# Kernel optimization log

Measured on AMD Instinct MI355X. Metric: run time of the kernel, lower is better.

The kernel has to match this reference:

```python
import jax, jax.numpy as jnp
import numpy as np
from jax import lax

RADIUS = 8
EPS = 1e-3
EPS_LOG = 1e-6
EPS_SCALE = 1e-4
A_COMP = 0.7
B_SHIFT = 0.0
DETAIL_GAIN = 1.0
DOWN = 0.5
# detail_threshold=0 and target_mean=0 -> those branches are inactive (defaults)

DN = (('NCHW', 'OIHW', 'NCHW'))


def _box_filter(x4d):
    """Separable box filter on [1,1,H,W] with reflect padding, kernel 2r+1."""
    k = 2 * RADIUS + 1
    xp = jnp.pad(x4d, ((0, 0), (0, 0), (RADIUS, RADIUS), (RADIUS, RADIUS)), mode='reflect')
    kh = jnp.full((1, 1, 1, k), 1.0 / k, dtype=x4d.dtype)
    kv = jnp.full((1, 1, k, 1), 1.0 / k, dtype=x4d.dtype)
    y = lax.conv_general_dilated(xp, kh, (1, 1), 'VALID', dimension_numbers=DN)
    y = lax.conv_general_dilated(y, kv, (1, 1), 'VALID', dimension_numbers=DN)
    return y


def _guided_filter(img):
    """Self-guided filter on a 2D image [H, W]."""
    x4 = img[None, None]
    mean_I = _box_filter(x4)
    mean_II = _box_filter(x4 * x4)
    var_I = mean_II - mean_I * mean_I
    a = var_I / (var_I + EPS)
    b = mean_I - a * mean_I
    out = _box_filter(a) * x4 + _box_filter(b)
    return out[0, 0]


def _bilinear_resize(img, oh, ow):
    """Bilinear resize [H,W] -> [oh,ow], half-pixel centers (align_corners=False),
    no antialias, matching torch F.interpolate(mode='bilinear')."""
    H, W = img.shape
    ys = jnp.maximum((jnp.arange(oh, dtype=img.dtype) + 0.5) * (H / oh) - 0.5, 0.0)
    xs = jnp.maximum((jnp.arange(ow, dtype=img.dtype) + 0.5) * (W / ow) - 0.5, 0.0)
    y0 = jnp.floor(ys)
    x0 = jnp.floor(xs)
    wy = (ys - y0)[:, None]
    wx = (xs - x0)[None, :]
    y0i = jnp.clip(y0.astype(jnp.int32), 0, H - 1)
    y1i = jnp.minimum(y0i + 1, H - 1)
    x0i = jnp.clip(x0.astype(jnp.int32), 0, W - 1)
    x1i = jnp.minimum(x0i + 1, W - 1)
    # vertical lerp, then horizontal lerp (separable)
    vert = img[y0i, :] * (1.0 - wy) + img[y1i, :] * wy       # [oh, W]
    out = vert[:, x0i] * (1.0 - wx) + vert[:, x1i] * wx      # [oh, ow]
    return out


def setup_inputs() -> dict:
    key = jax.random.key(0)
    x = jax.random.uniform(key, (2160, 3840, 3), dtype=jnp.float32)
    return {"x": x}


def reference(x) -> jnp.ndarray:
    H, W = x.shape[0], x.shape[1]
    Y = 0.2126 * x[..., 0] + 0.7152 * x[..., 1] + 0.0722 * x[..., 2]
    Y_log = jnp.log2(jnp.maximum(Y, EPS_LOG))
    # fast path: downsample -> guided filter -> upsample
    dh, dw = int(H * DOWN), int(W * DOWN)
    Y_log_down = _bilinear_resize(Y_log, dh, dw)
    Y_base_down = _guided_filter(Y_log_down)
    Y_base = _bilinear_resize(Y_base_down, H, W)
    Y_detail = Y_log - Y_base  # detail_threshold=0 -> no suppression
    Y_tm = (A_COMP * Y_base + B_SHIFT) + DETAIL_GAIN * Y_detail
    Y_out = jnp.exp2(Y_tm)
    scale = Y_out / (Y + EPS_SCALE)
    out = jnp.clip(x * scale[..., None], 0.0, 1.0)
    # target_mean=0 -> no global mean rescale
    return out
```

## Files before the change

kernel.cpp:

```cpp
#include <hip/hip_runtime.h>
#include <math.h>

#define H_FULL 2160
#define W_FULL 3840
#define H_D    1080
#define W_D    1920
#define KLEN   17
#define INV_K2 (1.0f/289.0f)

#if __has_builtin(__builtin_amdgcn_logf)
#define FAST_LOG2(x) __builtin_amdgcn_logf(x)
#else
#define FAST_LOG2(x) log2f(x)
#endif
#if __has_builtin(__builtin_amdgcn_exp2f)
#define FAST_EXP2(x) __builtin_amdgcn_exp2f(x)
#else
#define FAST_EXP2(x) exp2f(x)
#endif
#if __has_builtin(__builtin_amdgcn_rcpf)
#define FAST_RCP(x) __builtin_amdgcn_rcpf(x)
#else
#define FAST_RCP(x) (1.0f/(x))
#endif

static __device__ __forceinline__ int refl(int i, int n) {
    if (i < 0) i = -i;
    else if (i >= n) i = 2*n - 2 - i;
    return i;
}
static __device__ __forceinline__ float lum(float r, float g, float b) {
    return 0.2126f*r + 0.7152f*g + 0.0722f*b;
}
static __device__ __forceinline__ float lg(float y) {
    return FAST_LOG2(fmaxf(y, 1e-6f));
}

__global__ __launch_bounds__(256) void k_down(const float* __restrict__ x,
                                              float* __restrict__ I) {
    int t = blockIdx.x * 256 + threadIdx.x;
    int p = t * 2;
    int i = p / W_D;
    int j = p - i * W_D;
    const float4* r0 = (const float4*)(x + ((size_t)(2*i)   * W_FULL + 2*j) * 3);
    const float4* r1 = (const float4*)(x + ((size_t)(2*i+1) * W_FULL + 2*j) * 3);
    float4 a0 = r0[0], a1 = r0[1], a2 = r0[2];
    float4 b0 = r1[0], b1 = r1[1], b2 = r1[2];
    float y00 = lum(a0.x,a0.y,a0.z), y01 = lum(a0.w,a1.x,a1.y);
    float y02 = lum(a1.z,a1.w,a2.x), y03 = lum(a2.y,a2.z,a2.w);
    float y10 = lum(b0.x,b0.y,b0.z), y11 = lum(b0.w,b1.x,b1.y);
    float y12 = lum(b1.z,b1.w,b2.x), y13 = lum(b2.y,b2.z,b2.w);
    float o0 = 0.25f * (lg(y00)+lg(y01)+lg(y10)+lg(y11));
    float o1 = 0.25f * (lg(y02)+lg(y03)+lg(y12)+lg(y13));
    *(float2*)(I + (size_t)i * W_D + j) = make_float2(o0, o1);
}

__global__ __launch_bounds__(256) void k_ab(const float* __restrict__ I,
                                            float2* __restrict__ AB) {
    __shared__ float  sI[48 * 49];
    __shared__ float2 hs[48 * 33];
    int tx0 = blockIdx.x * 32;
    int ty0 = blockIdx.y * 32;
    int tid = threadIdx.x;

    for (int e = tid; e < 48 * 48; e += 256) {
        int r = e / 48, c = e - r * 48;
        sI[r * 49 + c] =
            I[(size_t)refl(ty0 - 8 + r, H_D) * W_D + refl(tx0 - 8 + c, W_D)];
    }
    __syncthreads();

    if (tid < 192) {
        int r = tid >> 2, run = tid & 3;
        int c0 = run * 8;
        const float* p = &sI[r * 49 + c0];
        float s1 = 0.f, s2 = 0.f;
        #pragma unroll
        for (int k = 0; k < KLEN; ++k) { float v = p[k]; s1 += v; s2 += v * v; }
        float2* o = &hs[r * 33 + c0];
        o[0] = make_float2(s1, s2);
        #pragma unroll
        for (int m = 1; m < 8; ++m) {
            float vo = p[m - 1], vi = p[m + 16];
            s1 += vi - vo;
            s2 += vi * vi - vo * vo;
            o[m] = make_float2(s1, s2);
        }
    }
    __syncthreads();

    if (tid < 128) {
        int c = tid & 31, run = tid >> 5;
        int r0 = run * 8;
        const float2* p = &hs[r0 * 33 + c];
        float s1 = 0.f, s2 = 0.f;
        #pragma unroll
        for (int k = 0; k < KLEN; ++k) { float2 v = p[k * 33]; s1 += v.x; s2 += v.y; }
        #pragma unroll
        for (int m = 0; m < 8; ++m) {
            if (m) {
                float2 vi = p[(m + 16) * 33], vo = p[(m - 1) * 33];
                s1 += vi.x - vo.x;
                s2 += vi.y - vo.y;
            }
            float mI  = s1 * INV_K2;
            float mII = s2 * INV_K2;
            float var = mII - mI * mI;
            float av  = var / (var + 1e-3f);
            int gr = ty0 + r0 + m;
            if (gr < H_D)
                AB[(size_t)gr * W_D + tx0 + c] = make_float2(av, mI - av * mI);
        }
    }
}

__global__ __launch_bounds__(512, 6) void k_fused2(const float* __restrict__ I,
                                                   const float2* __restrict__ AB,
                                                   const float* __restrict__ x,
                                                   float* __restrict__ out) {
    __shared__ char lds[39160];
    float2* sAB   = (float2*)(lds);
    float2* hAB   = (float2*)(lds + 20400);
    float*  sIc   = (float*) (lds + 34400);
    float*  baseL = (float*) (lds);

    int tx0 = blockIdx.x * 32;
    int ty0 = blockIdx.y * 32;
    int tid = threadIdx.x;

    for (int e = tid; e < 50 * 50; e += 512) {
        int r = e / 50, c = e - r * 50;
        sAB[r * 51 + c] =
            AB[(size_t)refl(ty0 - 9 + r, H_D) * W_D + refl(tx0 - 9 + c, W_D)];
    }
    for (int e = tid; e < 34 * 34; e += 512) {
        int r = e / 34, c = e - r * 34;
        sIc[r * 35 + c] =
            I[(size_t)refl(ty0 - 1 + r, H_D) * W_D + refl(tx0 - 1 + c, W_D)];
    }
    __syncthreads();

    if (tid < 200) {
        int r = tid % 50, run = tid / 50;
        int c0  = (run < 2) ? run * 9 : 18 + (run - 2) * 8;
        int len = (run < 2) ? 9 : 8;
        const float2* p = &sAB[r * 51 + c0];
        float sa = 0.f, sb = 0.f;
        #pragma unroll
        for (int k = 0; k < KLEN; ++k) { float2 v = p[k]; sa += v.x; sb += v.y; }
        float2* o = &hAB[r * 35 + c0];
        o[0] = make_float2(sa, sb);
        #pragma unroll
        for (int m = 1; m < 9; ++m) {
            if (m < len) {
                float2 vi = p[m + 16], vo = p[m - 1];
                sa += vi.x - vo.x;
                sb += vi.y - vo.y;
                o[m] = make_float2(sa, sb);
            }
        }
    }
    __syncthreads();

    if (tid < 136) {
        int cc = tid % 34, run = tid / 34;
        int r0  = (run < 2) ? run * 9 : 18 + (run - 2) * 8;
        int len = (run < 2) ? 9 : 8;
        const float2* p = &hAB[r0 * 35 + cc];
        float sa = 0.f, sb = 0.f;
        #pragma unroll
        for (int k = 0; k < KLEN; ++k) { float2 v = p[k * 35]; sa += v.x; sb += v.y; }
        #pragma unroll
        for (int m = 0; m < 9; ++m) {
            if (m < len) {
                if (m) {
                    float2 vi = p[(m + 16) * 35], vo = p[(m - 1) * 35];
                    sa += vi.x - vo.x;
                    sb += vi.y - vo.y;
                }
                int br = r0 + m;
                baseL[br * 35 + cc] =
                    (sa * INV_K2) * sIc[br * 35 + cc] + sb * INV_K2;
            }
        }
    }
    __syncthreads();

    int q  = tid & 15;
    int r  = tid >> 4;
    int j0 = tx0 * 2 + q * 4;
    int gc0 = tx0 + 2 * q - 1;
    int l0 = max(gc0, 0) - (tx0 - 1);
    int l1 = 2 * q + 1, l2 = 2 * q + 2;
    int l3 = min(gc0 + 3, W_D - 1) - (tx0 - 1);

    #pragma unroll
    for (int s = 0; s < 2; ++s) {
        int oy = ty0 * 2 + r + s * 32;
        if (oy < H_FULL) {
            int y0g = (oy - 1) >> 1;
            int ly0 = max(y0g, 0) - (ty0 - 1);
            int ly1 = min(y0g + 1, H_D - 1) - (ty0 - 1);
            float wy = (oy & 1) ? 0.25f : 0.75f;
            const float* b0r = &baseL[ly0 * 35];
            const float* b1r = &baseL[ly1 * 35];
            float v0 = b0r[l0] + (b1r[l0] - b0r[l0]) * wy;
            float v1 = b0r[l1] + (b1r[l1] - b0r[l1]) * wy;
            float v2 = b0r[l2] + (b1r[l2] - b0r[l2]) * wy;
            float v3 = b0r[l3] + (b1r[l3] - b0r[l3]) * wy;
            float Yb[4];
            Yb[0] = v0 + (v1 - v0) * 0.75f;
            Yb[1] = v1 + (v2 - v1) * 0.25f;
            Yb[2] = v1 + (v2 - v1) * 0.75f;
            Yb[3] = v2 + (v3 - v2) * 0.25f;

            size_t off = ((size_t)oy * W_FULL + j0) * 3;
            const float4* px = (const float4*)(x + off);
            float4 q0 = px[0], q1 = px[1], q2 = px[2];
            float rgb[12] = {q0.x,q0.y,q0.z,q0.w, q1.x,q1.y,q1.z,q1.w, q2.x,q2.y,q2.z,q2.w};
            float res[12];
            #pragma unroll
            for (int k = 0; k < 4; ++k) {
                float rr = rgb[3*k], gg = rgb[3*k+1], bb = rgb[3*k+2];
                float Y = lum(rr, gg, bb);
                float sc = fmaxf(Y, 1e-6f) * FAST_EXP2(-0.3f * Yb[k]) * FAST_RCP(Y + 1e-4f);
                res[3*k]   = fminf(fmaxf(rr * sc, 0.f), 1.f);
                res[3*k+1] = fminf(fmaxf(gg * sc, 0.f), 1.f);
                res[3*k+2] = fminf(fmaxf(bb * sc, 0.f), 1.f);
            }
            float4* po = (float4*)(out + off);
            po[0] = make_float4(res[0], res[1], res[2],  res[3]);
            po[1] = make_float4(res[4], res[5], res[6],  res[7]);
            po[2] = make_float4(res[8], res[9], res[10], res[11]);
        }
    }
}

__global__ __launch_bounds__(512, 6) void k_fused(const float* __restrict__ I,
                                                  const float* __restrict__ x,
                                                  float* __restrict__ out) {
    __shared__ char lds[52088];
    float*  sIc   = (float*) (lds);
    float*  sIf   = (float*) (lds + 4760);
    float2* ab    = (float2*)(lds + 4760);
    float2* hI    = (float2*)(lds + 25160);
    float2* hab   = (float2*)(lds + 25160);
    float*  baseL = (float*) (lds + 39160);

    int tx0 = blockIdx.x * 32;
    int ty0 = blockIdx.y * 32;
    int tid = threadIdx.x;

    for (int e = tid; e < 66 * 66; e += 512) {
        int r = e / 66, c = e - r * 66;
        sIf[r * 67 + c] =
            I[(size_t)refl(ty0 - 17 + r, H_D) * W_D + refl(tx0 - 17 + c, W_D)];
    }
    __syncthreads();

    if (tid < 330) {
        int r = tid / 5, run = tid - (tid / 5) * 5;
        int c0 = run * 10;
        const float* p = &sIf[r * 67 + c0];
        float s1 = 0.f, s2 = 0.f;
        #pragma unroll
        for (int k = 0; k < KLEN; ++k) { float v = p[k]; s1 += v; s2 += v * v; }
        float2* o = &hI[r * 51 + c0];
        o[0] = make_float2(s1, s2);
        #pragma unroll
        for (int m = 1; m < 10; ++m) {
            float vo = p[m - 1], vi = p[m + 16];
            s1 += vi - vo;
            s2 += vi * vi - vo * vo;
            o[m] = make_float2(s1, s2);
        }
    }
    for (int e = tid; e < 34 * 34; e += 512) {
        int r = e / 34, c = e - r * 34;
        sIc[r * 35 + c] = sIf[(r + 16) * 67 + (c + 16)];
    }
    __syncthreads();

    if (tid < 250) {
        int c = tid % 50, run = tid / 50;
        int r0 = run * 10;
        const float2* p = &hI[r0 * 51 + c];
        float s1 = 0.f, s2 = 0.f;
        #pragma unroll
        for (int k = 0; k < KLEN; ++k) { float2 v = p[k * 51]; s1 += v.x; s2 += v.y; }
        float2* o = &ab[r0 * 51 + c];
        #pragma unroll
        for (int m = 0; m < 10; ++m) {
            if (m) {
                float2 vi = p[(m + 16) * 51], vo = p[(m - 1) * 51];
                s1 += vi.x - vo.x;
                s2 += vi.y - vo.y;
            }
            float mI  = s1 * INV_K2;
            float mII = s2 * INV_K2;
            float var = mII - mI * mI;
            float av  = var / (var + 1e-3f);
            o[m * 51] = make_float2(av, mI - av * mI);
        }
    }
    __syncthreads();

    if (tid < 200) {
        int r = tid % 50, run = tid / 50;
        int c0  = (run < 2) ? run * 9 : 18 + (run - 2) * 8;
        int len = (run < 2) ? 9 : 8;
        const float2* p = &ab[r * 51 + c0];
        float sa = 0.f, sb = 0.f;
        #pragma unroll
        for (int k = 0; k < KLEN; ++k) { float2 v = p[k]; sa += v.x; sb += v.y; }
        float2* o = &hab[r * 35 + c0];
        o[0] = make_float2(sa, sb);
        #pragma unroll
        for (int m = 1; m < 9; ++m) {
            if (m < len) {
                float2 vi = p[m + 16], vo = p[m - 1];
                sa += vi.x - vo.x;
                sb += vi.y - vo.y;
                o[m] = make_float2(sa, sb);
            }
        }
    }
    __syncthreads();

    if (tid < 136) {
        int cc = tid % 34, run = tid / 34;
        int r0  = (run < 2) ? run * 9 : 18 + (run - 2) * 8;
        int len = (run < 2) ? 9 : 8;
        const float2* p = &hab[r0 * 35 + cc];
        float sa = 0.f, sb = 0.f;
        #pragma unroll
        for (int k = 0; k < KLEN; ++k) { float2 v = p[k * 35]; sa += v.x; sb += v.y; }
        #pragma unroll
        for (int m = 0; m < 9; ++m) {
            if (m < len) {
                if (m) {
                    float2 vi = p[(m + 16) * 35], vo = p[(m - 1) * 35];
                    sa += vi.x - vo.x;
                    sb += vi.y - vo.y;
                }
                int br = r0 + m;
                baseL[br * 35 + cc] =
                    (sa * INV_K2) * sIc[br * 35 + cc] + sb * INV_K2;
            }
        }
    }
    __syncthreads();

    int q  = tid & 15;
    int r  = tid >> 4;
    int j0 = tx0 * 2 + q * 4;
    int gc0 = tx0 + 2 * q - 1;
    int l0 = max(gc0, 0) - (tx0 - 1);
    int l1 = 2 * q + 1, l2 = 2 * q + 2;
    int l3 = min(gc0 + 3, W_D - 1) - (tx0 - 1);

    #pragma unroll
    for (int s = 0; s < 2; ++s) {
        int oy = ty0 * 2 + r + s * 32;
        if (oy < H_FULL) {
            int y0g = (oy - 1) >> 1;
            int ly0 = max(y0g, 0) - (ty0 - 1);
            int ly1 = min(y0g + 1, H_D - 1) - (ty0 - 1);
            float wy = (oy & 1) ? 0.25f : 0.75f;
            const float* b0r = &baseL[ly0 * 35];
            const float* b1r = &baseL[ly1 * 35];
            float v0 = b0r[l0] + (b1r[l0] - b0r[l0]) * wy;
            float v1 = b0r[l1] + (b1r[l1] - b0r[l1]) * wy;
            float v2 = b0r[l2] + (b1r[l2] - b0r[l2]) * wy;
            float v3 = b0r[l3] + (b1r[l3] - b0r[l3]) * wy;
            float Yb[4];
            Yb[0] = v0 + (v1 - v0) * 0.75f;
            Yb[1] = v1 + (v2 - v1) * 0.25f;
            Yb[2] = v1 + (v2 - v1) * 0.75f;
            Yb[3] = v2 + (v3 - v2) * 0.25f;

            size_t off = ((size_t)oy * W_FULL + j0) * 3;
            const float4* px = (const float4*)(x + off);
            float4 q0 = px[0], q1 = px[1], q2 = px[2];
            float rgb[12] = {q0.x,q0.y,q0.z,q0.w, q1.x,q1.y,q1.z,q1.w, q2.x,q2.y,q2.z,q2.w};
            float res[12];
            #pragma unroll
            for (int k = 0; k < 4; ++k) {
                float rr = rgb[3*k], gg = rgb[3*k+1], bb = rgb[3*k+2];
                float Y = lum(rr, gg, bb);
                float sc = fmaxf(Y, 1e-6f) * FAST_EXP2(-0.3f * Yb[k]) * FAST_RCP(Y + 1e-4f);
                res[3*k]   = fminf(fmaxf(rr * sc, 0.f), 1.f);
                res[3*k+1] = fminf(fmaxf(gg * sc, 0.f), 1.f);
                res[3*k+2] = fminf(fmaxf(bb * sc, 0.f), 1.f);
            }
            float4* po = (float4*)(out + off);
            po[0] = make_float4(res[0], res[1], res[2],  res[3]);
            po[1] = make_float4(res[4], res[5], res[6],  res[7]);
            po[2] = make_float4(res[8], res[9], res[10], res[11]);
        }
    }
}

extern "C" void kernel_launch(void* const* d_in, const int* in_sizes, int n_in,
                              void* d_out, int out_size, void* d_ws, size_t ws_size,
                              hipStream_t stream) {
    (void)in_sizes; (void)n_in; (void)out_size;
    const float* x = (const float*)d_in[0];
    float* out = (float*)d_out;
    float* I = (float*)d_ws;
    size_t plane = (size_t)H_D * W_D;

    if (ws_size >= plane * 12) {
        float2* AB = (float2*)(I + plane);
        k_down  <<<dim3(4050, 1, 1), dim3(256, 1, 1), 0, stream>>>(x, I);
        k_ab    <<<dim3(60, 34, 1),  dim3(256, 1, 1), 0, stream>>>(I, AB);
        k_fused2<<<dim3(60, 34, 1),  dim3(512, 1, 1), 0, stream>>>(I, AB, x, out);
    } else {
        k_down  <<<dim3(4050, 1, 1), dim3(256, 1, 1), 0, stream>>>(x, I);
        k_fused <<<dim3(60, 34, 1),  dim3(512, 1, 1), 0, stream>>>(I, x, out);
    }
}
```

Before: 77.96 us.

## Split fused base+tonemap kernel into separate base-filter and streaming tonemap kernels

Replaces k_fused2, which box-filtered a/b and applied tone mapping in one tile kernel, with two kernels. k_base computes the low-res base plane into workspace, and k_tm is a flat streaming kernel that upsamples base and tone-maps the full-res image. The aim is to take the LDS-heavy filter work off the bandwidth-bound full-res pass and let that pass run at higher occupancy with simple indexing. In exchange it adds a kernel launch, a low-res plane round trip through global memory, and a larger workspace requirement, so the fallback path triggers more easily.

```diff
diff --git a/kernel.cpp b/kernel.cpp
--- a/kernel.cpp
+++ b/kernel.cpp
@@ -114,29 +114,182 @@
     }
 }
 
-__global__ __launch_bounds__(512, 6) void k_fused2(const float* __restrict__ I,
-                                                   const float2* __restrict__ AB,
-                                                   const float* __restrict__ x,
-                                                   float* __restrict__ out) {
-    __shared__ char lds[39160];
-    float2* sAB   = (float2*)(lds);
-    float2* hAB   = (float2*)(lds + 20400);
-    float*  sIc   = (float*) (lds + 34400);
-    float*  baseL = (float*) (lds);
-
+__global__ __launch_bounds__(256) void k_base(const float2* __restrict__ AB,
+                                              const float* __restrict__ I,
+                                              float* __restrict__ base) {
+    __shared__ float2 sAB[48 * 49];
+    __shared__ float2 hs[48 * 33];
     int tx0 = blockIdx.x * 32;
     int ty0 = blockIdx.y * 32;
     int tid = threadIdx.x;
 
-    for (int e = tid; e < 50 * 50; e += 512) {
-        int r = e / 50, c = e - r * 50;
-        sAB[r * 51 + c] =
-            AB[(size_t)refl(ty0 - 9 + r, H_D) * W_D + refl(tx0 - 9 + c, W_D)];
+    for (int e = tid; e < 48 * 48; e += 256) {
+        int r = e / 48, c = e - r * 48;
+        sAB[r * 49 + c] =
+            AB[(size_t)refl(ty0 - 8 + r, H_D) * W_D + refl(tx0 - 8 + c, W_D)];
+    }
+    __syncthreads();
+
+    if (tid < 192) {
+        int r = tid >> 2, run = tid & 3;
+        int c0 = run * 8;
+        const float2* p = &sAB[r * 49 + c0];
+        float sa = 0.f, sb = 0.f;
+        #pragma unroll
+        for (int k = 0; k < KLEN; ++k) { float2 v = p[k]; sa += v.x; sb += v.y; }
+        float2* o = &hs[r * 33 + c0];
+        o[0] = make_float2(sa, sb);
+        #pragma unroll
+        for (int m = 1; m < 8; ++m) {
+            float2 vi = p[m + 16], vo = p[m - 1];
+            sa += vi.x - vo.x;
+            sb += vi.y - vo.y;
+            o[m] = make_float2(sa, sb);
+        }
+    }
+    __syncthreads();
+
+    if (tid < 128) {
+        int c = tid & 31, run = tid >> 5;
+        int r0 = run * 8;
+        const float2* p = &hs[r0 * 33 + c];
+        float sa = 0.f, sb = 0.f;
+        #pragma unroll
+        for (int k = 0; k < KLEN; ++k) { float2 v = p[k * 33]; sa += v.x; sb += v.y; }
+        int gc = tx0 + c;
+        #pragma unroll
+        for (int m = 0; m < 8; ++m) {
+            if (m) {
+                float2 vi = p[(m + 16) * 33], vo = p[(m - 1) * 33];
+                sa += vi.x - vo.x;
+                sb += vi.y - vo.y;
+            }
+            int gr = ty0 + r0 + m;
+            if (gr < H_D) {
+                float Ic = I[(size_t)gr * W_D + gc];
+                base[(size_t)gr * W_D + gc] = (sa * INV_K2) * Ic + sb * INV_K2;
+            }
+        }
+    }
+}
+
+__global__ __launch_bounds__(256) void k_tm(const float* __restrict__ x,
+                                            const float* __restrict__ base,
+                                            float* __restrict__ out) {
+    int t = blockIdx.x * 256 + threadIdx.x;
+    int oy = t / 960;
+    int g  = t - oy * 960;
+    int j0 = g * 4;
+    int k2 = g * 2;
+
+    int y0g = (oy - 1) >> 1;
+    int y0 = max(y0g, 0);
+    int y1 = min(y0g + 1, H_D - 1);
+    float wy = (oy & 1) ? 0.25f : 0.75f;
+    const float* b0 = base + (size_t)y0 * W_D;
+    const float* b1 = base + (size_t)y1 * W_D;
+    int c0 = max(k2 - 1, 0);
+    int c3 = min(k2 + 2, W_D - 1);
+    float u0 = b0[c0],     w0 = b1[c0];
+    float u1 = b0[k2],     w1 = b1[k2];
+    float u2 = b0[k2 + 1], w2 = b1[k2 + 1];
+    float u3 = b0[c3],     w3 = b1[c3];
+    float v0 = u0 + (w0 - u0) * wy;
+    float v1 = u1 + (w1 - u1) * wy;
+    float v2 = u2 + (w2 - u2) * wy;
+    float v3 = u3 + (w3 - u3) * wy;
+    float Yb[4];
+    Yb[0] = v0 + (v1 - v0) * 0.75f;
+    Yb[1] = v1 + (v2 - v1) * 0.25f;
+    Yb[2] = v1 + (v2 - v1) * 0.75f;
+    Yb[3] = v2 + (v3 - v2) * 0.25f;
+
+    size_t off = ((size_t)oy * W_FULL + j0) * 3;
+    const float4* px = (const float4*)(x + off);
+    float4 q0 = px[0], q1 = px[1], q2 = px[2];
+    float rgb[12] = {q0.x,q0.y,q0.z,q0.w, q1.x,q1.y,q1.z,q1.w, q2.x,q2.y,q2.z,q2.w};
+    float res[12];
+    #pragma unroll
+    for (int k = 0; k < 4; ++k) {
+        float rr = rgb[3*k], gg = rgb[3*k+1], bb = rgb[3*k+2];
+        float Y = lum(rr, gg, bb);
+        float sc = fmaxf(Y, 1e-6f) * FAST_EXP2(-0.3f * Yb[k]) * FAST_RCP(Y + 1e-4f);
+        res[3*k]   = fminf(fmaxf(rr * sc, 0.f), 1.f);
+        res[3*k+1] = fminf(fmaxf(gg * sc, 0.f), 1.f);
+        res[3*k+2] = fminf(fmaxf(bb * sc, 0.f), 1.f);
+    }
+    float4* po = (float4*)(out + off);
+    po[0] = make_float4(res[0], res[1], res[2],  res[3]);
+    po[1] = make_float4(res[4], res[5], res[6],  res[7]);
+    po[2] = make_float4(res[8], res[9], res[10], res[11]);
+}
+
+__global__ __launch_bounds__(512, 6) void k_fused(const float* __restrict__ I,
+                                                  const float* __restrict__ x,
+                                                  float* __restrict__ out) {
+    __shared__ char lds[52088];
+    float*  sIc   = (float*) (lds);
+    float*  sIf   = (float*) (lds + 4760);
+    float2* ab    = (float2*)(lds + 4760);
+    float2* hI    = (float2*)(lds + 25160);
+    float2* hab   = (float2*)(lds + 25160);
+    float*  baseL = (float*) (lds + 39160);
+
+    int tx0 = blockIdx.x * 32;
+    int ty0 = blockIdx.y * 32;
+    int tid = threadIdx.x;
+
+    for (int e = tid; e < 66 * 66; e += 512) {
+        int r = e / 66, c = e - r * 66;
+        sIf[r * 67 + c] =
+            I[(size_t)refl(ty0 - 17 + r, H_D) * W_D + refl(tx0 - 17 + c, W_D)];
+    }
+    __syncthreads();
+
+    if (tid < 330) {
+        int r = tid / 5, run = tid - (tid / 5) * 5;
+        int c0 = run * 10;
+        const float* p = &sIf[r * 67 + c0];
+        float s1 = 0.f, s2 = 0.f;
+        #pragma unroll
+        for (int k = 0; k < KLEN; ++k) { float v = p[k]; s1 += v; s2 += v * v; }
+        float2* o = &hI[r * 51 + c0];
+        o[0] = make_float2(s1, s2);
+        #pragma unroll
+        for (int m = 1; m < 10; ++m) {
+            float vo = p[m - 1], vi = p[m + 16];
+            s1 += vi - vo;
+            s2 += vi * vi - vo * vo;
+            o[m] = make_float2(s1, s2);
+        }
     }
     for (int e = tid; e < 34 * 34; e += 512) {
         int r = e / 34, c = e - r * 34;
-        sIc[r * 35 + c] =
-            I[(size_t)refl(ty0 - 1 + r, H_D) * W_D + refl(tx0 - 1 + c, W_D)];
+        sIc[r * 35 + c] = sIf[(r + 16) * 67 + (c + 16)];
+    }
+    __syncthreads();
+
+    if (tid < 250) {
+        int c = tid % 50, run = tid / 50;
+        int r0 = run * 10;
+        const float2* p = &hI[r0 * 51 + c];
+        float s1 = 0.f, s2 = 0.f;
+        #pragma unroll
+        for (int k = 0; k < KLEN; ++k) { float2 v = p[k * 51]; s1 += v.x; s2 += v.y; }
+        float2* o = &ab[r0 * 51 + c];
+        #pragma unroll
+        for (int m = 0; m < 10; ++m) {
+            if (m) {
+                float2 vi = p[(m + 16) * 51], vo = p[(m - 1) * 51];
+                s1 += vi.x - vo.x;
+                s2 += vi.y - vo.y;
+            }
+            float mI  = s1 * INV_K2;
+            float mII = s2 * INV_K2;
+            float var = mII - mI * mI;
+            float av  = var / (var + 1e-3f);
+            o[m * 51] = make_float2(av, mI - av * mI);
+        }
     }
     __syncthreads();
 
@@ -144,11 +297,11 @@
         int r = tid % 50, run = tid / 50;
         int c0  = (run < 2) ? run * 9 : 18 + (run - 2) * 8;
         int len = (run < 2) ? 9 : 8;
-        const float2* p = &sAB[r * 51 + c0];
+        const float2* p = &ab[r * 51 + c0];
         float sa = 0.f, sb = 0.f;
         #pragma unroll
         for (int k = 0; k < KLEN; ++k) { float2 v = p[k]; sa += v.x; sb += v.y; }
-        float2* o = &hAB[r * 35 + c0];
+        float2* o = &hab[r * 35 + c0];
         o[0] = make_float2(sa, sb);
         #pragma unroll
         for (int m = 1; m < 9; ++m) {
@@ -166,7 +319,7 @@
         int cc = tid % 34, run = tid / 34;
         int r0  = (run < 2) ? run * 9 : 18 + (run - 2) * 8;
         int len = (run < 2) ? 9 : 8;
-        const float2* p = &hAB[r0 * 35 + cc];
+        const float2* p = &hab[r0 * 35 + cc];
         float sa = 0.f, sb = 0.f;
         #pragma unroll
         for (int k = 0; k < KLEN; ++k) { float2 v = p[k * 35]; sa += v.x; sb += v.y; }
@@ -236,171 +389,6 @@
     }
 }
 
-__global__ __launch_bounds__(512, 6) void k_fused(const float* __restrict__ I,
-                                                  const float* __restrict__ x,
-                                                  float* __restrict__ out) {
-    __shared__ char lds[52088];
-    float*  sIc   = (float*) (lds);
-    float*  sIf   = (float*) (lds + 4760);
-    float2* ab    = (float2*)(lds + 4760);
-    float2* hI    = (float2*)(lds + 25160);
-    float2* hab   = (float2*)(lds + 25160);
-    float*  baseL = (float*) (lds + 39160);
-
-    int tx0 = blockIdx.x * 32;
-    int ty0 = blockIdx.y * 32;
-    int tid = threadIdx.x;
-
-    for (int e = tid; e < 66 * 66; e += 512) {
-        int r = e / 66, c = e - r * 66;
-        sIf[r * 67 + c] =
-            I[(size_t)refl(ty0 - 17 + r, H_D) * W_D + refl(tx0 - 17 + c, W_D)];
-    }
-    __syncthreads();
-
-    if (tid < 330) {
-        int r = tid / 5, run = tid - (tid / 5) * 5;
-        int c0 = run * 10;
-        const float* p = &sIf[r * 67 + c0];
-        float s1 = 0.f, s2 = 0.f;
-        #pragma unroll
-        for (int k = 0; k < KLEN; ++k) { float v = p[k]; s1 += v; s2 += v * v; }
-        float2* o = &hI[r * 51 + c0];
-        o[0] = make_float2(s1, s2);
-        #pragma unroll
-        for (int m = 1; m < 10; ++m) {
-            float vo = p[m - 1], vi = p[m + 16];
-            s1 += vi - vo;
-            s2 += vi * vi - vo * vo;
-            o[m] = make_float2(s1, s2);
-        }
-    }
-    for (int e = tid; e < 34 * 34; e += 512) {
-        int r = e / 34, c = e - r * 34;
-        sIc[r * 35 + c] = sIf[(r + 16) * 67 + (c + 16)];
-    }
-    __syncthreads();
-
-    if (tid < 250) {
-        int c = tid % 50, run = tid / 50;
-        int r0 = run * 10;
-        const float2* p = &hI[r0 * 51 + c];
-        float s1 = 0.f, s2 = 0.f;
-        #pragma unroll
-        for (int k = 0; k < KLEN; ++k) { float2 v = p[k * 51]; s1 += v.x; s2 += v.y; }
-        float2* o = &ab[r0 * 51 + c];
-        #pragma unroll
-        for (int m = 0; m < 10; ++m) {
-            if (m) {
-                float2 vi = p[(m + 16) * 51], vo = p[(m - 1) * 51];
-                s1 += vi.x - vo.x;
-                s2 += vi.y - vo.y;
-            }
-            float mI  = s1 * INV_K2;
-            float mII = s2 * INV_K2;
-            float var = mII - mI * mI;
-            float av  = var / (var + 1e-3f);
-            o[m * 51] = make_float2(av, mI - av * mI);
-        }
-    }
-    __syncthreads();
-
-    if (tid < 200) {
-        int r = tid % 50, run = tid / 50;
-        int c0  = (run < 2) ? run * 9 : 18 + (run - 2) * 8;
-        int len = (run < 2) ? 9 : 8;
-        const float2* p = &ab[r * 51 + c0];
-        float sa = 0.f, sb = 0.f;
-        #pragma unroll
-        for (int k = 0; k < KLEN; ++k) { float2 v = p[k]; sa += v.x; sb += v.y; }
-        float2* o = &hab[r * 35 + c0];
-        o[0] = make_float2(sa, sb);
-        #pragma unroll
-        for (int m = 1; m < 9; ++m) {
-            if (m < len) {
-                float2 vi = p[m + 16], vo = p[m - 1];
-                sa += vi.x - vo.x;
-                sb += vi.y - vo.y;
-                o[m] = make_float2(sa, sb);
-            }
-        }
-    }
-    __syncthreads();
-
-    if (tid < 136) {
-        int cc = tid % 34, run = tid / 34;
-        int r0  = (run < 2) ? run * 9 : 18 + (run - 2) * 8;
-        int len = (run < 2) ? 9 : 8;
-        const float2* p = &hab[r0 * 35 + cc];
-        float sa = 0.f, sb = 0.f;
-        #pragma unroll
-        for (int k = 0; k < KLEN; ++k) { float2 v = p[k * 35]; sa += v.x; sb += v.y; }
-        #pragma unroll
-        for (int m = 0; m < 9; ++m) {
-            if (m < len) {
-                if (m) {
-                    float2 vi = p[(m + 16) * 35], vo = p[(m - 1) * 35];
-                    sa += vi.x - vo.x;
-                    sb += vi.y - vo.y;
-                }
-                int br = r0 + m;
-                baseL[br * 35 + cc] =
-                    (sa * INV_K2) * sIc[br * 35 + cc] + sb * INV_K2;
-            }
-        }
-    }
-    __syncthreads();
-
-    int q  = tid & 15;
-    int r  = tid >> 4;
-    int j0 = tx0 * 2 + q * 4;
-    int gc0 = tx0 + 2 * q - 1;
-    int l0 = max(gc0, 0) - (tx0 - 1);
-    int l1 = 2 * q + 1, l2 = 2 * q + 2;
-    int l3 = min(gc0 + 3, W_D - 1) - (tx0 - 1);
-
-    #pragma unroll
-    for (int s = 0; s < 2; ++s) {
-        int oy = ty0 * 2 + r + s * 32;
-        if (oy < H_FULL) {
-            int y0g = (oy - 1) >> 1;
-            int ly0 = max(y0g, 0) - (ty0 - 1);
-            int ly1 = min(y0g + 1, H_D - 1) - (ty0 - 1);
-            float wy = (oy & 1) ? 0.25f : 0.75f;
-            const float* b0r = &baseL[ly0 * 35];
-            const float* b1r = &baseL[ly1 * 35];
-            float v0 = b0r[l0] + (b1r[l0] - b0r[l0]) * wy;
-            float v1 = b0r[l1] + (b1r[l1] - b0r[l1]) * wy;
-            float v2 = b0r[l2] + (b1r[l2] - b0r[l2]) * wy;
-            float v3 = b0r[l3] + (b1r[l3] - b0r[l3]) * wy;
-            float Yb[4];
-            Yb[0] = v0 + (v1 - v0) * 0.75f;
-            Yb[1] = v1 + (v2 - v1) * 0.25f;
-            Yb[2] = v1 + (v2 - v1) * 0.75f;
-            Yb[3] = v2 + (v3 - v2) * 0.25f;
-
-            size_t off = ((size_t)oy * W_FULL + j0) * 3;
-            const float4* px = (const float4*)(x + off);
-            float4 q0 = px[0], q1 = px[1], q2 = px[2];
-            float rgb[12] = {q0.x,q0.y,q0.z,q0.w, q1.x,q1.y,q1.z,q1.w, q2.x,q2.y,q2.z,q2.w};
-            float res[12];
-            #pragma unroll
-            for (int k = 0; k < 4; ++k) {
-                float rr = rgb[3*k], gg = rgb[3*k+1], bb = rgb[3*k+2];
-                float Y = lum(rr, gg, bb);
-                float sc = fmaxf(Y, 1e-6f) * FAST_EXP2(-0.3f * Yb[k]) * FAST_RCP(Y + 1e-4f);
-                res[3*k]   = fminf(fmaxf(rr * sc, 0.f), 1.f);
-                res[3*k+1] = fminf(fmaxf(gg * sc, 0.f), 1.f);
-                res[3*k+2] = fminf(fmaxf(bb * sc, 0.f), 1.f);
-            }
-            float4* po = (float4*)(out + off);
-            po[0] = make_float4(res[0], res[1], res[2],  res[3]);
-            po[1] = make_float4(res[4], res[5], res[6],  res[7]);
-            po[2] = make_float4(res[8], res[9], res[10], res[11]);
-        }
-    }
-}
-
 extern "C" void kernel_launch(void* const* d_in, const int* in_sizes, int n_in,
                               void* d_out, int out_size, void* d_ws, size_t ws_size,
                               hipStream_t stream) {
@@ -410,13 +398,15 @@
     float* I = (float*)d_ws;
     size_t plane = (size_t)H_D * W_D;
 
-    if (ws_size >= plane * 12) {
-        float2* AB = (float2*)(I + plane);
-        k_down  <<<dim3(4050, 1, 1), dim3(256, 1, 1), 0, stream>>>(x, I);
-        k_ab    <<<dim3(60, 34, 1),  dim3(256, 1, 1), 0, stream>>>(I, AB);
-        k_fused2<<<dim3(60, 34, 1),  dim3(512, 1, 1), 0, stream>>>(I, AB, x, out);
+    if (ws_size >= plane * 16) {
+        float2* AB   = (float2*)(I + plane);
+        float*  base = I + 3 * plane;
+        k_down<<<dim3(4050, 1, 1), dim3(256, 1, 1), 0, stream>>>(x, I);
+        k_ab  <<<dim3(60, 34, 1),  dim3(256, 1, 1), 0, stream>>>(I, AB);
+        k_base<<<dim3(60, 34, 1),  dim3(256, 1, 1), 0, stream>>>(AB, I, base);
+        k_tm  <<<dim3(8100, 1, 1), dim3(256, 1, 1), 0, stream>>>(x, base, out);
     } else {
-        k_down  <<<dim3(4050, 1, 1), dim3(256, 1, 1), 0, stream>>>(x, I);
-        k_fused <<<dim3(60, 34, 1),  dim3(512, 1, 1), 0, stream>>>(I, x, out);
-    }
-}
+        k_down <<<dim3(4050, 1, 1), dim3(256, 1, 1), 0, stream>>>(x, I);
+        k_fused<<<dim3(60, 34, 1),  dim3(512, 1, 1), 0, stream>>>(I, x, out);
+    }
+}
```

Measured after the change: 86.52 us. 1.11x slower.
